# Kernel tuning notes

Measured on AMD Instinct MI355X. Metric: run time of the kernel, lower is better.

Reference implementation:

```python
import jax, jax.numpy as jnp
import numpy as np

N = 50000
E = 800000
F_IN = 128
H = 128
C = 16


def _balanced_conv(x, row, col, W, b, num_nodes):
    # x: [N, in] -> linear -> gather(row) * norm -> scatter-add(col) + bias
    x = x @ W  # [N, out]
    deg = jax.ops.segment_sum(jnp.ones(row.shape[0], x.dtype), col,
                              num_segments=num_nodes)  # includes self-loops -> deg >= 1
    dinv = deg ** -0.5
    norm = dinv[row] * dinv[col]  # [E+N]
    msg = norm[:, None] * x[row]  # gather + scale
    out = jax.ops.segment_sum(msg, col, num_segments=num_nodes)  # scatter-add
    return out + b


def setup_inputs() -> dict:
    key = jax.random.key(0)
    ks = jax.random.split(key, 12)
    x = jax.random.normal(ks[0], (N, F_IN), dtype=jnp.float32)
    edge_index = jax.random.randint(ks[1], (2, E), 0, N, dtype=jnp.int64)
    s = 1.0 / np.sqrt(F_IN)
    sh = 1.0 / np.sqrt(H)
    return {
        "x": x,
        "edge_index": edge_index,
        "importance": jnp.ones((F_IN,), jnp.float32),
        "W1": jax.random.uniform(ks[2], (F_IN, H), jnp.float32, -s, s),
        "b1": jnp.zeros((H,), jnp.float32),
        "W2": jax.random.uniform(ks[3], (H, H), jnp.float32, -sh, sh),
        "b2": jnp.zeros((H,), jnp.float32),
        "W3": jax.random.uniform(ks[4], (H, H), jnp.float32, -sh, sh),
        "b3": jnp.zeros((H,), jnp.float32),
        "lw1": jax.random.uniform(ks[5], (H, H), jnp.float32, -sh, sh),
        "lb1": jax.random.uniform(ks[6], (H,), jnp.float32, -sh, sh),
        "lw2": jax.random.uniform(ks[7], (H, C), jnp.float32, -sh, sh),
        "lb2": jax.random.uniform(ks[8], (C,), jnp.float32, -sh, sh),
    }


def reference(x, edge_index, importance, W1, b1, W2, b2, W3, b3, lw1, lb1, lw2, lb2):
    num_nodes = x.shape[0]
    # add self-loops (static shape: E + N)
    loops = jnp.arange(num_nodes, dtype=edge_index.dtype)
    row = jnp.concatenate([edge_index[0], loops])
    col = jnp.concatenate([edge_index[1], loops])

    gelu = lambda t: jax.nn.gelu(t, approximate=False)  # torch F.gelu default = erf

    h = x * importance  # FeatureImportance
    h = gelu(_balanced_conv(h, row, col, W1, b1, num_nodes))
    h = gelu(_balanced_conv(h, row, col, W2, b2, num_nodes))
    h = gelu(_balanced_conv(h, row, col, W3, b3, num_nodes))
    h = gelu(h @ lw1 + lb1)
    return h @ lw2 + lb2  # [N, C]
```

## Files before the change

kernel.cpp:

```cpp
#include <hip/hip_runtime.h>
#include <math.h>

#define NNODES 50000
#define NEDGES 800000
#define FDIM 128
#define NBUCKET 196
#define BCAP 6144
#define ABLK 261
#define EPWA 3072
#define MGRID 782

typedef unsigned short ushortT;
typedef unsigned int uintT;
typedef __attribute__((ext_vector_type(8))) short short8;
typedef __attribute__((ext_vector_type(4))) float floatx4;

__device__ __forceinline__ float gelu_erf(float x){
    return 0.5f * x * (1.0f + erff(x * 0.70710678118654752f));
}
__device__ __forceinline__ float bflo(uintT u){ return __uint_as_float(u << 16); }
__device__ __forceinline__ float bfhi(uintT u){ return __uint_as_float(u & 0xFFFF0000u); }
__device__ __forceinline__ ushortT f2bf(float f){
    uintT u = __float_as_uint(f);
    return (ushortT)((u + 0x7FFFu + ((u >> 16) & 1u)) >> 16);
}
__device__ __forceinline__ void split_bf16(float f, ushortT& hi, ushortT& lo){
    uintT u = __float_as_uint(f);
    hi = (ushortT)(u >> 16);
    float fhi = __uint_as_float(u & 0xFFFF0000u);
    lo = (ushortT)(__float_as_uint(f - fhi) >> 16);
}

__global__ void k_zero(int* __restrict__ gcur){
    if (threadIdx.x < NBUCKET) gcur[threadIdx.x] = 0;
}

__global__ __launch_bounds__(256) void k_bucketA(const int* __restrict__ ei,
                                                 int* __restrict__ gcur,
                                                 uintT* __restrict__ bucket){
    __shared__ int hist[NBUCKET];
    __shared__ int base[NBUCKET];
    int t = threadIdx.x;
    if (t < NBUCKET) hist[t] = 0;
    __syncthreads();
    int e0 = blockIdx.x * EPWA;
    int cr_c[12], cr_r[12];
    #pragma unroll
    for (int p = 0; p < 12; p++){
        int e = e0 + p*256 + t;
        if (e < NEDGES){
            cr_r[p] = ei[e];
            cr_c[p] = ei[NEDGES + e];
            atomicAdd(&hist[cr_c[p] >> 8], 1);
        } else cr_c[p] = -1;
    }
    __syncthreads();
    if (t < NBUCKET){
        base[t] = atomicAdd(&gcur[t], hist[t]);
        hist[t] = 0;
    }
    __syncthreads();
    #pragma unroll
    for (int p = 0; p < 12; p++){
        int c = cr_c[p];
        if (c >= 0){
            int b = c >> 8;
            int lp = atomicAdd(&hist[b], 1);
            bucket[(size_t)b*BCAP + base[b] + lp] = ((uintT)c << 16) | (uintT)cr_r[p];
        }
    }
}

__global__ __launch_bounds__(256) void k_bucketB(const int* __restrict__ gcur,
                                                 const uintT* __restrict__ bucket,
                                                 int* __restrict__ offs,
                                                 float* __restrict__ dinv,
                                                 ushortT* __restrict__ csr2){
    __shared__ int sm[256];
    __shared__ int hist[256];
    __shared__ int lcur[256];
    int b = blockIdx.x;
    int t = threadIdx.x;
    int n0 = b << 8;

    int gv = (t < NBUCKET) ? gcur[t] : 0;
    sm[t] = gv;
    __syncthreads();
    for (int off = 1; off < 256; off <<= 1){
        int tv = (t >= off) ? sm[t-off] : 0;
        __syncthreads();
        sm[t] += tv;
        __syncthreads();
    }
    __shared__ int bbase_s;
    if (t == b) bbase_s = sm[t] - gv;
    hist[t] = 0;
    __syncthreads();
    int bbase = bbase_s;
    int count = gcur[b];
    const uintT* src = bucket + (size_t)b*BCAP;

    for (int i = t; i < count; i += 256)
        atomicAdd(&hist[(src[i] >> 16) & 255], 1);
    __syncthreads();

    int v = hist[t];
    sm[t] = v;
    __syncthreads();
    for (int off = 1; off < 256; off <<= 1){
        int tv = (t >= off) ? sm[t-off] : 0;
        __syncthreads();
        sm[t] += tv;
        __syncthreads();
    }
    int excl = bbase + sm[t] - v;
    int node = n0 + t;
    if (node <= NNODES) offs[node] = excl;
    if (node < NNODES) dinv[node] = rsqrtf((float)(v + 1));
    if (b == NBUCKET-1 && t == 255) offs[NNODES] = NEDGES;
    lcur[t] = excl;
    __syncthreads();

    for (int i = t; i < count; i += 256){
        uintT e = src[i];
        int pos = atomicAdd(&lcur[(e >> 16) & 255], 1);
        csr2[pos] = (ushortT)(e & 0xFFFFu);
    }
}

__global__ __launch_bounds__(256) void k_packW(const float* __restrict__ Wa,
                                               const float* __restrict__ Wb,
                                               const float* __restrict__ Wc,
                                               const float* __restrict__ Wd,
                                               ushortT* __restrict__ Wp){
    int l = blockIdx.x;
    const float* W = (l==0) ? Wa : (l==1) ? Wb : (l==2) ? Wc : Wd;
    ushortT* hiP = Wp + (size_t)l*2*16384;
    ushortT* loP = hiP + 16384;
    for (int idx = threadIdx.x; idx < 16384; idx += 256){
        int k = idx >> 7, n = idx & 127;
        ushortT hi, lo;
        split_bf16(W[idx], hi, lo);
        int kc = k >> 5, quad = (k >> 3) & 3, j = k & 7;
        int nt = n >> 4, lane = (n & 15) + (quad << 4);
        int off = ((kc*8 + nt)*64 + lane)*8 + j;
        hiP[off] = hi;
        loP[off] = lo;
    }
}

template<int OUTMODE>
__global__ __launch_bounds__(256) void k_mfma(const float* __restrict__ A,
                                              const ushortT* __restrict__ Wp,
                                              const float* __restrict__ scale,
                                              const float* __restrict__ dinv,
                                              const float* __restrict__ bias,
                                              void* __restrict__ Yout){
    __shared__ float As[64*132];
    int t = threadIdx.x;
    int wave = t >> 6, lane = t & 63;
    int r = lane & 15, quad = lane >> 4;
    int row0 = blockIdx.x*64;
    int m0 = row0 + wave*16;
    const ushortT* WpLo = Wp + 16384;

    #pragma unroll
    for (int p = 0; p < 8; p++){
        int idx = p*256 + t;
        int rr = idx >> 5;
        int c4 = idx & 31;
        int gr = row0 + rr;
        float4 v = make_float4(0.f,0.f,0.f,0.f);
        if (gr < NNODES) v = *(const float4*)&A[(size_t)gr*FDIM + c4*4];
        if (scale){
            float4 s = *(const float4*)&scale[c4*4];
            v.x*=s.x; v.y*=s.y; v.z*=s.z; v.w*=s.w;
        }
        *(float4*)&As[rr*132 + c4*4] = v;
    }
    __syncthreads();

    floatx4 acc[8];
    #pragma unroll
    for (int nt = 0; nt < 8; nt++) acc[nt] = (floatx4){0.f,0.f,0.f,0.f};

    int arl = wave*16 + r;
    #pragma unroll
    for (int kc = 0; kc < 4; kc++){
        int kb = kc*32 + quad*8;
        float4 a0 = *(const float4*)&As[arl*132 + kb];
        float4 a1 = *(const float4*)&As[arl*132 + kb + 4];
        float av[8] = {a0.x, a0.y, a0.z, a0.w, a1.x, a1.y, a1.z, a1.w};
        short8 ahi, alo;
        #pragma unroll
        for (int e = 0; e < 8; e++){
            ushortT h, l;
            split_bf16(av[e], h, l);
            ahi[e] = (short)h;
            alo[e] = (short)l;
        }
        #pragma unroll
        for (int nt = 0; nt < 8; nt++){
            size_t boff = (size_t)(((kc*8 + nt)*64 + lane))*8;
            short8 bhi = *(const short8*)&Wp[boff];
            short8 blo = *(const short8*)&WpLo[boff];
            acc[nt] = __builtin_amdgcn_mfma_f32_16x16x32_bf16(ahi, bhi, acc[nt], 0, 0, 0);
            acc[nt] = __builtin_amdgcn_mfma_f32_16x16x32_bf16(alo, bhi, acc[nt], 0, 0, 0);
            acc[nt] = __builtin_amdgcn_mfma_f32_16x16x32_bf16(ahi, blo, acc[nt], 0, 0, 0);
        }
    }

    int orow0 = m0 + quad*4;
    if (OUTMODE == 1){
        float4 dv = *(const float4*)&dinv[orow0];
        float dva[4] = {dv.x, dv.y, dv.z, dv.w};
        ushortT* Yb = (ushortT*)Yout;
        #pragma unroll
        for (int nt = 0; nt < 8; nt++){
            int n = nt*16 + r;
            int chunk = n >> 5, o = n & 31;
            #pragma unroll
            for (int reg = 0; reg < 4; reg++){
                int orow = orow0 + reg;
                if (orow < NNODES){
                    float v = acc[nt][reg] * dva[reg];
                    __builtin_nontemporal_store(f2bf(v),
                        &Yb[((size_t)chunk*NNODES + orow)*32 + o]);
                }
            }
        }
    } else {
        float* Yf = (float*)Yout;
        #pragma unroll
        for (int nt = 0; nt < 8; nt++){
            int n = nt*16 + r;
            float bv = bias[n];
            #pragma unroll
            for (int reg = 0; reg < 4; reg++){
                int orow = orow0 + reg;
                if (orow < NNODES){
                    Yf[(size_t)orow*FDIM + n] = gelu_erf(acc[nt][reg] + bv);
                }
            }
        }
    }
}

__global__ __launch_bounds__(256) void k_aggregate(const ushortT* __restrict__ Yt,
                                                   const float* __restrict__ dinv,
                                                   const int* __restrict__ offs,
                                                   const ushortT* __restrict__ csr2,
                                                   const float* __restrict__ bias,
                                                   float* __restrict__ Hout){
    int bid = blockIdx.x;
    int chunk = bid & 3;
    int node = (bid >> 2) * 16 + (threadIdx.x >> 4);
    int lane = threadIdx.x & 15;
    const uintT* Yc = (const uintT*)Yt + (size_t)chunk * NNODES * 16;

    uintT a0 = Yc[node*16 + lane];
    float2 acc;
    acc.x = bflo(a0);
    acc.y = bfhi(a0);
    int e0 = offs[node], e1 = offs[node+1];
    int e = e0;
    for (; e + 7 < e1; e += 8){
        int r0 = csr2[e+0];
        int r1 = csr2[e+1];
        int r2 = csr2[e+2];
        int r3 = csr2[e+3];
        int r4 = csr2[e+4];
        int r5 = csr2[e+5];
        int r6 = csr2[e+6];
        int r7 = csr2[e+7];
        uintT q0 = Yc[r0*16 + lane];
        uintT q1 = Yc[r1*16 + lane];
        uintT q2 = Yc[r2*16 + lane];
        uintT q3 = Yc[r3*16 + lane];
        uintT q4 = Yc[r4*16 + lane];
        uintT q5 = Yc[r5*16 + lane];
        uintT q6 = Yc[r6*16 + lane];
        uintT q7 = Yc[r7*16 + lane];
        acc.x += bflo(q0); acc.y += bfhi(q0);
        acc.x += bflo(q1); acc.y += bfhi(q1);
        acc.x += bflo(q2); acc.y += bfhi(q2);
        acc.x += bflo(q3); acc.y += bfhi(q3);
        acc.x += bflo(q4); acc.y += bfhi(q4);
        acc.x += bflo(q5); acc.y += bfhi(q5);
        acc.x += bflo(q6); acc.y += bfhi(q6);
        acc.x += bflo(q7); acc.y += bfhi(q7);
    }
    for (; e + 1 < e1; e += 2){
        int r0 = csr2[e], r1 = csr2[e+1];
        uintT q0 = Yc[r0*16 + lane];
        uintT q1 = Yc[r1*16 + lane];
        acc.x += bflo(q0); acc.y += bfhi(q0);
        acc.x += bflo(q1); acc.y += bfhi(q1);
    }
    if (e < e1){
        uintT q = Yc[csr2[e]*16 + lane];
        acc.x += bflo(q); acc.y += bfhi(q);
    }
    float dc = dinv[node];
    float2 bv = ((const float2*)bias)[chunk*16 + lane];
    acc.x = gelu_erf(fmaf(dc, acc.x, bv.x));
    acc.y = gelu_erf(fmaf(dc, acc.y, bv.y));
    float* dst = &Hout[(size_t)node*FDIM + chunk*32 + lane*2];
    __builtin_nontemporal_store(acc.x, dst);
    __builtin_nontemporal_store(acc.y, dst+1);
}

__global__ __launch_bounds__(256) void k_gemm16(const float* __restrict__ A,
                                                const float* __restrict__ W,
                                                const float* __restrict__ bias,
                                                float* __restrict__ out){
    __shared__ float Hs[16][132];
    __shared__ float Ws2[128][16];
    int row0 = blockIdx.x * 16;
    int t = threadIdx.x;
    #pragma unroll
    for (int p=0;p<8;p++){
        int lin = p*256 + t;
        int r = lin >> 7, c = lin & 127;
        Hs[r][c] = A[(row0+r)*FDIM + c];
    }
    #pragma unroll
    for (int p=0;p<8;p++){
        int lin = p*256 + t;
        Ws2[lin>>4][lin&15] = W[lin];
    }
    __syncthreads();
    int il = t >> 4, j = t & 15;
    float acc = bias[j];
    #pragma unroll
    for (int k=0;k<FDIM;k++) acc = fmaf(Hs[il][k], Ws2[k][j], acc);
    out[(row0+il)*16 + j] = acc;
}

extern "C" void kernel_launch(void* const* d_in, const int* in_sizes, int n_in,
                              void* d_out, int out_size, void* d_ws, size_t ws_size,
                              hipStream_t stream) {
    const float* x    = (const float*)d_in[0];
    const int*   ei   = (const int*)d_in[1];
    const float* imp  = (const float*)d_in[2];
    const float* W1   = (const float*)d_in[3];
    const float* b1   = (const float*)d_in[4];
    const float* W2   = (const float*)d_in[5];
    const float* b2   = (const float*)d_in[6];
    const float* W3   = (const float*)d_in[7];
    const float* b3   = (const float*)d_in[8];
    const float* lw1  = (const float*)d_in[9];
    const float* lb1  = (const float*)d_in[10];
    const float* lw2  = (const float*)d_in[11];
    const float* lb2  = (const float*)d_in[12];
    float* out = (float*)d_out;

    int*   offs   = (int*)d_ws;
    int*   gcur   = (int*)d_ws + 50048;
    float* dinv   = (float*)d_ws + 50304;
    ushortT* csr2 = (ushortT*)((int*)d_ws + 100480);
    uintT* bucket = (uintT*)((int*)d_ws + 500480);
    ushortT* Wp   = (ushortT*)((int*)d_ws + 1704704);
    ushortT* bufYt= (ushortT*)((int*)d_ws + 1770240);
    float* bufY   = (float*)d_ws + 1770240;
    float* bufH   = (float*)d_ws + 8170240;

    dim3 B(256);
    k_packW  <<<4, B, 0, stream>>>(W1, W2, W3, lw1, Wp);
    k_zero   <<<1, B, 0, stream>>>(gcur);
    k_bucketA<<<ABLK, B, 0, stream>>>(ei, gcur, bucket);
    k_bucketB<<<NBUCKET, B, 0, stream>>>(gcur, bucket, offs, dinv, csr2);

    k_mfma<1><<<MGRID, B, 0, stream>>>(x,    Wp + 0*32768, imp,     dinv, nullptr, (void*)bufYt);
    k_aggregate<<<(NNODES/16)*4, B, 0, stream>>>(bufYt, dinv, offs, csr2, b1, bufH);
    k_mfma<1><<<MGRID, B, 0, stream>>>(bufH, Wp + 1*32768, nullptr, dinv, nullptr, (void*)bufYt);
    k_aggregate<<<(NNODES/16)*4, B, 0, stream>>>(bufYt, dinv, offs, csr2, b2, bufH);
    k_mfma<1><<<MGRID, B, 0, stream>>>(bufH, Wp + 2*32768, nullptr, dinv, nullptr, (void*)bufYt);
    k_aggregate<<<(NNODES/16)*4, B, 0, stream>>>(bufYt, dinv, offs, csr2, b3, bufH);

    k_mfma<0><<<MGRID, B, 0, stream>>>(bufH, Wp + 3*32768, nullptr, nullptr, lb1, (void*)bufY);
    k_gemm16<<<NNODES/16, B, 0, stream>>>(bufY, lw2, lb2, out);
}
```

Measured before the change: 346.7 us.

## Store intermediate activations in bf16 and drop LDS staging in later GEMMs

Hidden activations between layers are now written as packed bf16 instead of fp32, which halves the write traffic in aggregation and the read traffic in the GEMMs. Layers 2-4 use a new GEMM kernel that loads bf16 A fragments straight from global memory with no shared-memory staging or hi/lo split, so it issues two MFMAs per tile instead of three. The first layer keeps the fp32 path with the importance scale. The risk is lower precision on the activations, since the A operand is no longer split into hi/lo parts.

```diff
diff --git a/kernel.cpp b/kernel.cpp
--- a/kernel.cpp
+++ b/kernel.cpp
@@ -149,13 +149,11 @@
     }
 }
 
-template<int OUTMODE>
-__global__ __launch_bounds__(256) void k_mfma(const float* __restrict__ A,
-                                              const ushortT* __restrict__ Wp,
-                                              const float* __restrict__ scale,
-                                              const float* __restrict__ dinv,
-                                              const float* __restrict__ bias,
-                                              void* __restrict__ Yout){
+__global__ __launch_bounds__(256) void k_mfma_f32(const float* __restrict__ A,
+                                                  const ushortT* __restrict__ Wp,
+                                                  const float* __restrict__ scale,
+                                                  const float* __restrict__ dinv,
+                                                  ushortT* __restrict__ Yb){
     __shared__ float As[64*132];
     int t = threadIdx.x;
     int wave = t >> 6, lane = t & 63;
@@ -172,10 +170,8 @@
         int gr = row0 + rr;
         float4 v = make_float4(0.f,0.f,0.f,0.f);
         if (gr < NNODES) v = *(const float4*)&A[(size_t)gr*FDIM + c4*4];
-        if (scale){
-            float4 s = *(const float4*)&scale[c4*4];
-            v.x*=s.x; v.y*=s.y; v.z*=s.z; v.w*=s.w;
-        }
+        float4 s = *(const float4*)&scale[c4*4];
+        v.x*=s.x; v.y*=s.y; v.z*=s.z; v.w*=s.w;
         *(float4*)&As[rr*132 + c4*4] = v;
     }
     __syncthreads();
@@ -211,10 +207,63 @@
     }
 
     int orow0 = m0 + quad*4;
+    float4 dv = *(const float4*)&dinv[orow0];
+    float dva[4] = {dv.x, dv.y, dv.z, dv.w};
+    #pragma unroll
+    for (int nt = 0; nt < 8; nt++){
+        int n = nt*16 + r;
+        int chunk = n >> 5, o = n & 31;
+        #pragma unroll
+        for (int reg = 0; reg < 4; reg++){
+            int orow = orow0 + reg;
+            if (orow < NNODES){
+                float v = acc[nt][reg] * dva[reg];
+                __builtin_nontemporal_store(f2bf(v),
+                    &Yb[((size_t)chunk*NNODES + orow)*32 + o]);
+            }
+        }
+    }
+}
+
+template<int OUTMODE>
+__global__ __launch_bounds__(256) void k_mfma_b16(const ushortT* __restrict__ Ab,
+                                                  const ushortT* __restrict__ Wp,
+                                                  const float* __restrict__ dinv,
+                                                  const float* __restrict__ bias,
+                                                  ushortT* __restrict__ Yb){
+    int t = threadIdx.x;
+    int wave = t >> 6, lane = t & 63;
+    int r = lane & 15, quad = lane >> 4;
+    int m0 = blockIdx.x*64 + wave*16;
+    int arow = m0 + r;
+    if (arow >= NNODES) arow = NNODES - 1;
+    const ushortT* WpLo = Wp + 16384;
+
+    floatx4 acc[8];
+    #pragma unroll
+    for (int nt = 0; nt < 8; nt++) acc[nt] = (floatx4){0.f,0.f,0.f,0.f};
+
+    short8 afr[4];
+    #pragma unroll
+    for (int kc = 0; kc < 4; kc++)
+        afr[kc] = *(const short8*)&Ab[(size_t)arow*FDIM + kc*32 + quad*8];
+
+    #pragma unroll
+    for (int kc = 0; kc < 4; kc++){
+        #pragma unroll
+        for (int nt = 0; nt < 8; nt++){
+            size_t boff = (size_t)(((kc*8 + nt)*64 + lane))*8;
+            short8 bhi = *(const short8*)&Wp[boff];
+            short8 blo = *(const short8*)&WpLo[boff];
+            acc[nt] = __builtin_amdgcn_mfma_f32_16x16x32_bf16(afr[kc], bhi, acc[nt], 0, 0, 0);
+            acc[nt] = __builtin_amdgcn_mfma_f32_16x16x32_bf16(afr[kc], blo, acc[nt], 0, 0, 0);
+        }
+    }
+
+    int orow0 = m0 + quad*4;
     if (OUTMODE == 1){
         float4 dv = *(const float4*)&dinv[orow0];
         float dva[4] = {dv.x, dv.y, dv.z, dv.w};
-        ushortT* Yb = (ushortT*)Yout;
         #pragma unroll
         for (int nt = 0; nt < 8; nt++){
             int n = nt*16 + r;
@@ -230,7 +279,6 @@
             }
         }
     } else {
-        float* Yf = (float*)Yout;
         #pragma unroll
         for (int nt = 0; nt < 8; nt++){
             int n = nt*16 + r;
@@ -239,7 +287,8 @@
             for (int reg = 0; reg < 4; reg++){
                 int orow = orow0 + reg;
                 if (orow < NNODES){
-                    Yf[(size_t)orow*FDIM + n] = gelu_erf(acc[nt][reg] + bv);
+                    float v = gelu_erf(acc[nt][reg] + bv);
+                    __builtin_nontemporal_store(f2bf(v), &Yb[(size_t)orow*FDIM + n]);
                 }
             }
         }
@@ -251,7 +300,7 @@
                                                    const int* __restrict__ offs,
                                                    const ushortT* __restrict__ csr2,
                                                    const float* __restrict__ bias,
-                                                   float* __restrict__ Hout){
+                                                   ushortT* __restrict__ Hout){
     int bid = blockIdx.x;
     int chunk = bid & 3;
     int node = (bid >> 2) * 16 + (threadIdx.x >> 4);
@@ -305,12 +354,12 @@
     float2 bv = ((const float2*)bias)[chunk*16 + lane];
     acc.x = gelu_erf(fmaf(dc, acc.x, bv.x));
     acc.y = gelu_erf(fmaf(dc, acc.y, bv.y));
-    float* dst = &Hout[(size_t)node*FDIM + chunk*32 + lane*2];
-    __builtin_nontemporal_store(acc.x, dst);
-    __builtin_nontemporal_store(acc.y, dst+1);
-}
-
-__global__ __launch_bounds__(256) void k_gemm16(const float* __restrict__ A,
+    uintT packed = (uintT)f2bf(acc.x) | ((uintT)f2bf(acc.y) << 16);
+    uintT* dst = (uintT*)&Hout[(size_t)node*FDIM + chunk*32 + lane*2];
+    __builtin_nontemporal_store(packed, dst);
+}
+
+__global__ __launch_bounds__(256) void k_gemm16(const ushortT* __restrict__ A,
                                                 const float* __restrict__ W,
                                                 const float* __restrict__ bias,
                                                 float* __restrict__ out){
@@ -318,11 +367,14 @@
     __shared__ float Ws2[128][16];
     int row0 = blockIdx.x * 16;
     int t = threadIdx.x;
-    #pragma unroll
-    for (int p=0;p<8;p++){
-        int lin = p*256 + t;
-        int r = lin >> 7, c = lin & 127;
-        Hs[r][c] = A[(row0+r)*FDIM + c];
+    const uintT* A2 = (const uintT*)A;
+    #pragma unroll
+    for (int p=0;p<4;p++){
+        int idx = p*256 + t;
+        int r = idx >> 6, c2 = idx & 63;
+        uintT u = A2[(size_t)(row0+r)*64 + c2];
+        Hs[r][c2*2]   = bflo(u);
+        Hs[r][c2*2+1] = bfhi(u);
     }
     #pragma unroll
     for (int p=0;p<8;p++){
@@ -362,8 +414,8 @@
     uintT* bucket = (uintT*)((int*)d_ws + 500480);
     ushortT* Wp   = (ushortT*)((int*)d_ws + 1704704);
     ushortT* bufYt= (ushortT*)((int*)d_ws + 1770240);
-    float* bufY   = (float*)d_ws + 1770240;
-    float* bufH   = (float*)d_ws + 8170240;
+    ushortT* bufPb= bufYt;
+    ushortT* bufH = (ushortT*)((int*)d_ws + 8170240);
 
     dim3 B(256);
     k_packW  <<<4, B, 0, stream>>>(W1, W2, W3, lw1, Wp);
@@ -371,13 +423,13 @@
     k_bucketA<<<ABLK, B, 0, stream>>>(ei, gcur, bucket);
     k_bucketB<<<NBUCKET, B, 0, stream>>>(gcur, bucket, offs, dinv, csr2);
 
-    k_mfma<1><<<MGRID, B, 0, stream>>>(x,    Wp + 0*32768, imp,     dinv, nullptr, (void*)bufYt);
-    k_aggregate<<<(NNODES/16)*4, B, 0, stream>>>(bufYt, dinv, offs, csr2, b1, bufH);
-    k_mfma<1><<<MGRID, B, 0, stream>>>(bufH, Wp + 1*32768, nullptr, dinv, nullptr, (void*)bufYt);
-    k_aggregate<<<(NNODES/16)*4, B, 0, stream>>>(bufYt, dinv, offs, csr2, b2, bufH);
-    k_mfma<1><<<MGRID, B, 0, stream>>>(bufH, Wp + 2*32768, nullptr, dinv, nullptr, (void*)bufYt);
-    k_aggregate<<<(NNODES/16)*4, B, 0, stream>>>(bufYt, dinv, offs, csr2, b3, bufH);
-
-    k_mfma<0><<<MGRID, B, 0, stream>>>(bufH, Wp + 3*32768, nullptr, nullptr, lb1, (void*)bufY);
-    k_gemm16<<<NNODES/16, B, 0, stream>>>(bufY, lw2, lb2, out);
-}
+    k_mfma_f32  <<<MGRID, B, 0, stream>>>(x, Wp + 0*32768, imp, dinv, bufYt);
+    k_aggregate <<<(NNODES/16)*4, B, 0, stream>>>(bufYt, dinv, offs, csr2, b1, bufH);
+    k_mfma_b16<1><<<MGRID, B, 0, stream>>>(bufH, Wp + 1*32768, dinv, nullptr, bufYt);
+    k_aggregate <<<(NNODES/16)*4, B, 0, stream>>>(bufYt, dinv, offs, csr2, b2, bufH);
+    k_mfma_b16<1><<<MGRID, B, 0, stream>>>(bufH, Wp + 2*32768, dinv, nullptr, bufYt);
+    k_aggregate <<<(NNODES/16)*4, B, 0, stream>>>(bufYt, dinv, offs, csr2, b3, bufH);
+
+    k_mfma_b16<0><<<MGRID, B, 0, stream>>>(bufH, Wp + 3*32768, nullptr, lb1, bufPb);
+    k_gemm16<<<NNODES/16, B, 0, stream>>>(bufPb, lw2, lb2, out);
+}
```

New measurement: 339.8 us. 2.0% less time.
